# Kernel tuning notes

Measured on AMD Instinct MI355X. Metric: run time of the kernel, lower is better.

Reference implementation:

```python
import jax, jax.numpy as jnp
import numpy as np

N_HEADS, N_LEVELS, N_POINTS = 8, 4, 4
D_MODEL, D_FFN = 256, 2048
NQ, BS = 900, 4
SPATIAL = np.array([[128, 128], [64, 64], [32, 32], [16, 16]], dtype=np.int64)
HW = int((SPATIAL[:, 0] * SPATIAL[:, 1]).sum())


def _ln(x, g, b):
    mu = x.mean(-1, keepdims=True)
    var = x.var(-1, keepdims=True)
    return (x - mu) / jnp.sqrt(var + 1e-5) * g + b


def _lin(x, w, b):
    return x @ w.T + b


def _msdeform_attn(query, refp, mem, ss, starts, so_w, so_b, aw_w, aw_b, vp_w, vp_b, op_w, op_b):
    # query: (bs, nq, d), refp: (bs, nq, L, 2) in [0,1], mem: (bs, hw, d)
    bs, nq, d = query.shape
    hd = d // N_HEADS
    value = _lin(mem, vp_w, vp_b).reshape(bs, -1, N_HEADS, hd)  # (bs, hw, H, hd)
    offsets = _lin(query, so_w, so_b).reshape(bs, nq, N_HEADS, N_LEVELS, N_POINTS, 2)
    aw = _lin(query, aw_w, aw_b).reshape(bs, nq, N_HEADS, N_LEVELS * N_POINTS)
    aw = jax.nn.softmax(aw, axis=-1).reshape(bs, nq, N_HEADS, N_LEVELS, N_POINTS)
    # offset normalizer is (W, H) per level
    normalizer = jnp.asarray(ss[:, ::-1].copy(), dtype=query.dtype)  # (L, 2)
    loc = refp[:, :, None, :, None, :] + offsets / normalizer[None, None, None, :, None, :]
    out = jnp.zeros((bs, nq, N_HEADS, hd), dtype=query.dtype)
    for l in range(N_LEVELS):
        h_l, w_l = int(ss[l, 0]), int(ss[l, 1])
        vl = value[:, starts[l]:starts[l] + h_l * w_l]  # (bs, h*w, H, hd)
        # grid_sample align_corners=False: pixel coord = loc*size - 0.5
        x = loc[:, :, :, l, :, 0] * w_l - 0.5  # (bs, nq, H, P)
        y = loc[:, :, :, l, :, 1] * h_l - 0.5
        x0 = jnp.floor(x)
        y0 = jnp.floor(y)
        fx = x - x0
        fy = y - y0

        def gather(ix, iy, wgt):
            valid = (ix >= 0) & (ix < w_l) & (iy >= 0) & (iy < h_l)
            idx = (jnp.clip(iy, 0, h_l - 1) * w_l + jnp.clip(ix, 0, w_l - 1)).astype(jnp.int32)
            # (bs, nq, H, P) -> (bs, nq*P, H) to match vl's (bs, hw, H, hd)
            idxt = idx.transpose(0, 1, 3, 2).reshape(bs, nq * N_POINTS, N_HEADS)
            g = jnp.take_along_axis(vl, idxt[..., None], axis=1)  # (bs, nq*P, H, hd)
            g = g.reshape(bs, nq, N_POINTS, N_HEADS, hd).transpose(0, 1, 3, 2, 4)
            return g * (wgt * valid)[..., None]

        x0i = x0.astype(jnp.int32)
        y0i = y0.astype(jnp.int32)
        sampled = (gather(x0i, y0i, (1 - fx) * (1 - fy))
                   + gather(x0i + 1, y0i, fx * (1 - fy))
                   + gather(x0i, y0i + 1, (1 - fx) * fy)
                   + gather(x0i + 1, y0i + 1, fx * fy))  # (bs, nq, H, P, hd)
        out = out + (sampled * aw[:, :, :, l, :, None]).sum(axis=3)
    return _lin(out.reshape(bs, nq, d), op_w, op_b)


def _fwd(tgt, query_pos, memory, ref_points,
         sa_in_w, sa_in_b, sa_out_w, sa_out_b,
         ln1_g, ln1_b, ln2_g, ln2_b, ln3_g, ln3_b,
         so_w, so_b, aw_w, aw_b, vp_w, vp_b, op_w, op_b,
         ff1_w, ff1_b, ff2_w, ff2_b, spatial_shapes, level_start_index):
    nq, bs, d = tgt.shape
    hd = d // N_HEADS
    ss = np.asarray(spatial_shapes)
    starts = np.asarray(level_start_index)
    # ---- self attention (q = k = tgt + pos, v = tgt) ----
    qk = tgt + query_pos
    q = _lin(qk, sa_in_w[:d], sa_in_b[:d]).reshape(nq, bs, N_HEADS, hd)
    k = _lin(qk, sa_in_w[d:2 * d], sa_in_b[d:2 * d]).reshape(nq, bs, N_HEADS, hd)
    v = _lin(tgt, sa_in_w[2 * d:], sa_in_b[2 * d:]).reshape(nq, bs, N_HEADS, hd)
    scores = jnp.einsum('qbhd,kbhd->bhqk', q, k) / np.sqrt(hd).astype(tgt.dtype)
    attn = jax.nn.softmax(scores, axis=-1)
    sa = jnp.einsum('bhqk,kbhd->qbhd', attn, v).reshape(nq, bs, d)
    sa = _lin(sa, sa_out_w, sa_out_b)
    tgt = _ln(tgt + sa, ln2_g, ln2_b)
    # ---- deformable cross attention ----
    ca = _msdeform_attn((tgt + query_pos).transpose(1, 0, 2),
                        ref_points.transpose(1, 0, 2, 3),
                        memory.transpose(1, 0, 2), ss, starts,
                        so_w, so_b, aw_w, aw_b, vp_w, vp_b, op_w, op_b)
    tgt = _ln(tgt + ca.transpose(1, 0, 2), ln1_g, ln1_b)
    # ---- FFN ----
    ff = _lin(jax.nn.relu(_lin(tgt, ff1_w, ff1_b)), ff2_w, ff2_b)
    return _ln(tgt + ff, ln3_g, ln3_b)


def setup_inputs() -> dict:
    key = jax.random.key(0)
    ks = iter(jax.random.split(key, 32))
    d, dffn = D_MODEL, D_FFN
    nofs = N_HEADS * N_LEVELS * N_POINTS
    w = lambda *s: jax.random.normal(next(ks), s, dtype=jnp.float32) * 0.02
    starts = np.concatenate([[0], np.cumsum(SPATIAL[:, 0] * SPATIAL[:, 1])[:-1]]).astype(np.int64)
    return {
        'tgt': jax.random.normal(next(ks), (NQ, BS, d), dtype=jnp.float32),
        'query_pos': jax.random.normal(next(ks), (NQ, BS, d), dtype=jnp.float32),
        'memory': jax.random.normal(next(ks), (HW, BS, d), dtype=jnp.float32),
        'ref_points': jax.random.uniform(next(ks), (NQ, BS, N_LEVELS, 2), dtype=jnp.float32),
        'sa_in_w': w(3 * d, d), 'sa_in_b': w(3 * d), 'sa_out_w': w(d, d), 'sa_out_b': w(d),
        'ln1_g': jnp.ones((d,)), 'ln1_b': jnp.zeros((d,)),
        'ln2_g': jnp.ones((d,)), 'ln2_b': jnp.zeros((d,)),
        'ln3_g': jnp.ones((d,)), 'ln3_b': jnp.zeros((d,)),
        'so_w': w(nofs * 2, d), 'so_b': jax.random.normal(next(ks), (nofs * 2,), dtype=jnp.float32) * 0.5,
        'aw_w': w(nofs, d), 'aw_b': w(nofs),
        'vp_w': w(d, d), 'vp_b': w(d), 'op_w': w(d, d), 'op_b': w(d),
        'ff1_w': w(dffn, d), 'ff1_b': w(dffn), 'ff2_w': w(d, dffn), 'ff2_b': w(d),
        'spatial_shapes': SPATIAL, 'level_start_index': starts,
    }


def reference(tgt, query_pos, memory, ref_points, sa_in_w, sa_in_b, sa_out_w, sa_out_b, ln1_g, ln1_b, ln2_g, ln2_b, ln3_g, ln3_b, so_w, so_b, aw_w, aw_b, vp_w, vp_b, op_w, op_b, ff1_w, ff1_b, ff2_w, ff2_b, spatial_shapes, level_start_index):
    return _fwd(tgt, query_pos, memory, ref_points, sa_in_w, sa_in_b, sa_out_w, sa_out_b,
                ln1_g, ln1_b, ln2_g, ln2_b, ln3_g, ln3_b, so_w, so_b, aw_w, aw_b,
                vp_w, vp_b, op_w, op_b, ff1_w, ff1_b, ff2_w, ff2_b,
                spatial_shapes, level_start_index)
```

## Files before the change

kernel.cpp:

```cpp
#include <hip/hip_runtime.h>
#include <hip/hip_bf16.h>

#define D_MODEL 256
#define N_HEADS 8
#define HD 32
#define NQ 900
#define BS 4
#define MROWS (NQ * BS)
#define HW_TOT 21760
#define VROWS (HW_TOT * BS)

typedef __attribute__((ext_vector_type(8))) short bf16x8;
typedef __attribute__((ext_vector_type(4))) float f32x4;

__device__ inline short f2b(float f) {
  union { __hip_bfloat16 h; short s; } u;
  u.h = __float2bfloat16(f);
  return u.s;
}
__device__ inline float bu2f(unsigned short u) {
  union { unsigned int i; float f; } c;
  c.i = ((unsigned int)u) << 16;
  return c.f;
}
__device__ inline bf16x8 bzero8() {
  bf16x8 v;
#pragma unroll
  for (int j = 0; j < 8; ++j) v[j] = 0;
  return v;
}
__device__ inline f32x4 fzero4() {
  f32x4 v;
#pragma unroll
  for (int j = 0; j < 4; ++j) v[j] = 0.f;
  return v;
}

#define GLL16(gsrc, ldst)                                                     \
  __builtin_amdgcn_global_load_lds(                                           \
      (__attribute__((address_space(1))) void*)(gsrc),                        \
      (__attribute__((address_space(3))) void*)(ldst), 16, 0, 0)

__global__ __launch_bounds__(256) void prep_all(const float* __restrict__ s0,
                                                const float* __restrict__ s1,
                                                const float* __restrict__ s2,
                                                const float* __restrict__ s3,
                                                const float* __restrict__ s4,
                                                const float* __restrict__ s5,
                                                const float* __restrict__ s6,
                                                const float* __restrict__ s7,
                                                short* __restrict__ dst,
                                                const float* __restrict__ tgt,
                                                const float* __restrict__ qpos,
                                                short* __restrict__ tgtb,
                                                short* __restrict__ qkb,
                                                const float* __restrict__ so_b,
                                                const float* __restrict__ aw_b,
                                                float* __restrict__ biasSOAW) {
  int i = blockIdx.x * 256 + threadIdx.x;
  if (i < 1540096) {
    const float* s; int off;
    if (i < 196608)      { s = s0; off = 0; }
    else if (i < 262144) { s = s1; off = 196608; }
    else if (i < 327680) { s = s2; off = 262144; }
    else if (i < 360448) { s = s3; off = 327680; }
    else if (i < 425984) { s = s4; off = 360448; }
    else if (i < 491520) { s = s5; off = 425984; }
    else if (i < 1015808){ s = s6; off = 491520; }
    else                 { s = s7; off = 1015808; }
    dst[i] = f2b(s[i - off]);
  } else {
    int j = i - 1540096;
    float t = tgt[j], p = qpos[j];
    tgtb[j] = f2b(t);
    qkb[j] = f2b(t + p);
    if (j < 384) biasSOAW[j] = (j < 256) ? so_b[j] : aw_b[j - 256];
  }
}

template <int BN, int AF32, int OUTF32, int RELU>
__device__ __forceinline__ void gemm_core(const void* __restrict__ Xv,
                                          const short* __restrict__ W,
                                          const float* __restrict__ bias,
                                          void* __restrict__ outv,
                                          int M, int N, int K, int m0, int n0,
                                          int t0, int t1, int addBias,
                                          short* __restrict__ smem) {
  constexpr int NF = BN / 16;
  short* sA = smem;
  short* sB = smem + 2 * 2048;
  const int tid = threadIdx.x;
  const int wave = tid >> 6, lane = tid & 63;
  const int l15 = lane & 15, l4 = lane >> 4;
  const int wr = wave * 16;
  const float* Xf = (const float*)Xv;
  const short* Xh = (const short*)Xv;

  f32x4 acc[NF];
#pragma unroll
  for (int f = 0; f < NF; ++f) acc[f] = fzero4();

  const int alr = wave * 16 + (lane >> 2);
  const int ags = (lane & 3) ^ ((alr >> 1) & 3);
  const int arow = tid >> 2, ak = tid & 3;
  const int agsrc = ak ^ ((arow >> 1) & 3);
  float4 ra0, ra1;

  auto stageB = [&](int t, int buf) {
    short* bb = sB + buf * BN * 32;
#pragma unroll
    for (int j = 0; j < BN / 64; ++j) {
      int lr = j * 64 + alr;
      int gs = (lane & 3) ^ ((lr >> 1) & 3);
      const short* src = W + (size_t)(n0 + lr) * K + t * 32 + gs * 8;
      GLL16(src, bb + (j * 64 + wave * 16) * 32);
    }
  };
  auto stageA_gll = [&](int t, int buf) {
    const short* src = Xh + (size_t)(m0 + alr) * K + t * 32 + ags * 8;
    GLL16(src, sA + buf * 2048 + wave * 512);
  };
  auto loadA_f32 = [&](int t) {
    const float* p = Xf + (size_t)(m0 + arow) * K + t * 32 + agsrc * 8;
    ra0 = *reinterpret_cast<const float4*>(p);
    ra1 = *reinterpret_cast<const float4*>(p + 4);
  };
  auto writeA_f32 = [&](int buf) {
    bf16x8 v;
    v[0] = f2b(ra0.x); v[1] = f2b(ra0.y); v[2] = f2b(ra0.z); v[3] = f2b(ra0.w);
    v[4] = f2b(ra1.x); v[5] = f2b(ra1.y); v[6] = f2b(ra1.z); v[7] = f2b(ra1.w);
    *reinterpret_cast<bf16x8*>(&sA[buf * 2048 + arow * 32 + ak * 8]) = v;
  };
  auto compute = [&](int buf) {
    const int r = wr + l15;
    bf16x8 av = *reinterpret_cast<const bf16x8*>(
        &sA[buf * 2048 + r * 32 + ((l4 ^ ((r >> 1) & 3)) * 8)]);
#pragma unroll
    for (int f = 0; f < NF; ++f) {
      const int rb = f * 16 + l15;
      bf16x8 bv = *reinterpret_cast<const bf16x8*>(
          &sB[buf * BN * 32 + rb * 32 + ((l4 ^ ((rb >> 1) & 3)) * 8)]);
      acc[f] = __builtin_amdgcn_mfma_f32_16x16x32_bf16(av, bv, acc[f], 0, 0, 0);
    }
  };

  if constexpr (AF32) { loadA_f32(t0); writeA_f32(0); }
  else stageA_gll(t0, 0);
  stageB(t0, 0);
  __syncthreads();

  int buf = 0;
  for (int t = t0; t < t1; ++t) {
    if (t + 1 < t1) {
      if constexpr (AF32) loadA_f32(t + 1);
      else stageA_gll(t + 1, buf ^ 1);
      stageB(t + 1, buf ^ 1);
    }
    compute(buf);
    if (AF32 && t + 1 < t1) writeA_f32(buf ^ 1);
    __syncthreads();
    buf ^= 1;
  }

#pragma unroll
  for (int f = 0; f < NF; ++f) {
    int col = n0 + f * 16 + l15;
    float bfv = addBias ? bias[col] : 0.f;
#pragma unroll
    for (int i = 0; i < 4; ++i) {
      int row = m0 + wr + l4 * 4 + i;
      if (row >= M) continue;
      float v = acc[f][i] + bfv;
      if (RELU) v = fmaxf(v, 0.f);
      if constexpr (OUTF32)
        ((float*)outv)[(size_t)row * N + col] = v;
      else
        ((short*)outv)[(size_t)row * N + col] = f2b(v);
    }
  }
}

template <int BN, int AF32, int OUTF32, int RELU>
__global__ __launch_bounds__(256) void gemm2(const void* __restrict__ Xv,
                                             const short* __restrict__ W,
                                             const float* __restrict__ bias,
                                             void* __restrict__ outv,
                                             int M, int N, int K) {
  __shared__ __align__(16) short smem[2 * 2048 + 2 * BN * 32];
  gemm_core<BN, AF32, OUTF32, RELU>(Xv, W, bias, outv, M, N, K,
                                    blockIdx.x * 64, blockIdx.y * BN,
                                    0, K / 32, 1, smem);
}

__global__ __launch_bounds__(256) void gemm_splitk(const void* __restrict__ Xv,
                                                   const short* __restrict__ W,
                                                   const float* __restrict__ bias,
                                                   float* __restrict__ outp,
                                                   int M, int N, int K) {
  __shared__ __align__(16) short smem[2 * 2048 + 2 * 64 * 32];
  const int kc = blockIdx.z;
  const int ntc = K / 32 / 4;
  gemm_core<64, 0, 1, 0>(Xv, W, bias, outp + (size_t)kc * M * N, M, N, K,
                         blockIdx.x * 64, blockIdx.y * 64,
                         kc * ntc, (kc + 1) * ntc, kc == 0, smem);
}

__global__ __launch_bounds__(256) void qkv_gemm(const short* __restrict__ qkb,
                                                const short* __restrict__ tgtb,
                                                const short* __restrict__ Wqkv,
                                                const float* __restrict__ sa_in_b,
                                                short* __restrict__ QKb,
                                                short* __restrict__ Vb) {
  __shared__ __align__(16) short smem[2 * 2048 + 2 * 64 * 32];
  int bx = blockIdx.x;
  if (bx < 456) {
    gemm_core<64, 0, 0, 0>(qkb, Wqkv, sa_in_b, QKb, MROWS, 512, 256,
                           (bx % 57) * 64, (bx / 57) * 64, 0, 8, 1, smem);
  } else {
    bx -= 456;
    gemm_core<64, 0, 0, 0>(tgtb, Wqkv + 512 * 256, sa_in_b + 512, Vb, MROWS, 256, 256,
                           (bx % 57) * 64, (bx / 57) * 64, 0, 8, 1, smem);
  }
}

__device__ __forceinline__ void flash_body(const short* __restrict__ QK,
                                           const short* __restrict__ V,
                                           short* __restrict__ O,
                                           int bid, short* __restrict__ smem) {
  const int bh = bid & 31, b = bh >> 3, h = bh & 7;
  const int q0 = (bid >> 5) * 64;
  const int tid = threadIdx.x, wave = tid >> 6, lane = tid & 63;
  const int l15 = lane & 15, l4 = lane >> 4;
  const int cb = h * 32;

  short* sQ = smem;
  short* sK = smem + 2560;
  short* sVt = smem + 5120;
  short* sP = smem + 7424;

  {
    int row = tid >> 2, kof = (tid & 3) * 8;
    int q = q0 + row;
    bf16x8 v = (q < NQ) ? *reinterpret_cast<const bf16x8*>(QK + (size_t)(q * 4 + b) * 512 + cb + kof)
                        : bzero8();
    *reinterpret_cast<bf16x8*>(&sQ[row * 40 + kof]) = v;
  }
  __syncthreads();
  const int wr = wave * 16;
  const bf16x8 aq = *reinterpret_cast<bf16x8*>(&sQ[(wr + l15) * 40 + l4 * 8]);

  float mrow[4], lrow[4];
#pragma unroll
  for (int i = 0; i < 4; ++i) { mrow[i] = -1e30f; lrow[i] = 0.f; }
  f32x4 accO[2];
  accO[0] = fzero4(); accO[1] = fzero4();

  const int pswz = (((wr >> 2) + l4) & 3) << 3;
  const int pswzr = (((wr >> 2) + (l15 >> 2)) & 3) << 3;

  for (int kt = 0; kt < 15; ++kt) {
    const int k0 = kt * 64;
    {
      int row = tid >> 2, kof = (tid & 3) * 8;
      int kk = k0 + row;
      bf16x8 v = (kk < NQ)
          ? *reinterpret_cast<const bf16x8*>(QK + (size_t)(kk * 4 + b) * 512 + 256 + cb + kof)
          : bzero8();
      *reinterpret_cast<bf16x8*>(&sK[row * 40 + kof]) = v;
    }
    {
      int row = tid >> 2, dof = (tid & 3) * 8;
      int kk = k0 + row;
      bf16x8 vv = (kk < NQ)
          ? *reinterpret_cast<const bf16x8*>(V + (size_t)(kk * 4 + b) * 256 + cb + dof)
          : bzero8();
      const int kp = row ^ (((dof >> 3) & 3) << 4);
#pragma unroll
      for (int j = 0; j < 8; ++j) sVt[(dof + j) * 72 + kp] = vv[j];
    }
    __syncthreads();

    f32x4 s[4];
#pragma unroll
    for (int f = 0; f < 4; ++f) {
      bf16x8 bk = *reinterpret_cast<bf16x8*>(&sK[(f * 16 + l15) * 40 + l4 * 8]);
      s[f] = __builtin_amdgcn_mfma_f32_16x16x32_bf16(aq, bk, fzero4(), 0, 0, 0);
    }
#pragma unroll
    for (int f = 0; f < 4; ++f) {
      bool valid = (k0 + f * 16 + l15) < NQ;
#pragma unroll
      for (int i = 0; i < 4; ++i) {
        float sv = s[f][i] * 0.17677669529663687f;
        s[f][i] = valid ? sv : -1e30f;
      }
    }
    float mx[4];
#pragma unroll
    for (int i = 0; i < 4; ++i)
      mx[i] = fmaxf(fmaxf(s[0][i], s[1][i]), fmaxf(s[2][i], s[3][i]));
#pragma unroll
    for (int off = 1; off < 16; off <<= 1)
#pragma unroll
      for (int i = 0; i < 4; ++i) mx[i] = fmaxf(mx[i], __shfl_xor(mx[i], off));

    float alpha[4], rs[4];
#pragma unroll
    for (int i = 0; i < 4; ++i) {
      float mn = fmaxf(mrow[i], mx[i]);
      alpha[i] = __expf(mrow[i] - mn);
      mrow[i] = mn;
      rs[i] = 0.f;
    }
#pragma unroll
    for (int f = 0; f < 4; ++f)
#pragma unroll
      for (int i = 0; i < 4; ++i) {
        float p = __expf(s[f][i] - mrow[i]);
        rs[i] += p;
        sP[(wr + l4 * 4 + i) * 72 + ((f * 16 + l15) ^ pswz)] = f2b(p);
      }
#pragma unroll
    for (int off = 1; off < 16; off <<= 1)
#pragma unroll
      for (int i = 0; i < 4; ++i) rs[i] += __shfl_xor(rs[i], off);
#pragma unroll
    for (int i = 0; i < 4; ++i) lrow[i] = lrow[i] * alpha[i] + rs[i];
#pragma unroll
    for (int nf = 0; nf < 2; ++nf)
#pragma unroll
      for (int i = 0; i < 4; ++i) accO[nf][i] *= alpha[i];

#pragma unroll
    for (int ks = 0; ks < 2; ++ks) {
      bf16x8 ap = *reinterpret_cast<bf16x8*>(&sP[(wr + l15) * 72 + ((ks * 32 + l4 * 8) ^ pswzr)]);
#pragma unroll
      for (int nf = 0; nf < 2; ++nf) {
        const int d = nf * 16 + l15;
        const int kb = (ks * 32 + l4 * 8) ^ (((d >> 3) & 3) << 4);
        bf16x8 bv = *reinterpret_cast<bf16x8*>(&sVt[d * 72 + kb]);
        accO[nf] = __builtin_amdgcn_mfma_f32_16x16x32_bf16(ap, bv, accO[nf], 0, 0, 0);
      }
    }
    __syncthreads();
  }

#pragma unroll
  for (int nf = 0; nf < 2; ++nf)
#pragma unroll
    for (int i = 0; i < 4; ++i) {
      int q = q0 + wr + l4 * 4 + i;
      if (q < NQ)
        O[(size_t)(q * 4 + b) * 256 + cb + nf * 16 + l15] = f2b(accO[nf][i] / lrow[i]);
    }
}

__global__ __launch_bounds__(256) void flash_value(const short* __restrict__ QKb,
                                                   const short* __restrict__ Vb,
                                                   short* __restrict__ Ob,
                                                   const float* __restrict__ memory,
                                                   const short* __restrict__ Wvp,
                                                   const float* __restrict__ vp_b,
                                                   short* __restrict__ value) {
  __shared__ __align__(16) short smem[2 * 2048 + 2 * 128 * 32];
  int bx = blockIdx.x;
  if (bx < 480) {
    flash_body(QKb, Vb, Ob, bx, smem);
  } else {
    bx -= 480;
    gemm_core<128, 1, 0, 0>(memory, Wvp, vp_b, value, VROWS, 256, 256,
                            (bx >> 1) * 64, (bx & 1) * 128, 0, 8, 1, smem);
  }
}

__global__ __launch_bounds__(256) void ln_kernel(const float* __restrict__ A,
                                                 const float* __restrict__ B,
                                                 const float* __restrict__ g,
                                                 const float* __restrict__ bb,
                                                 float* __restrict__ outF,
                                                 short* __restrict__ outB,
                                                 const float* __restrict__ addv) {
  const int row = blockIdx.x;
  const int t = threadIdx.x;
  const size_t base = (size_t)row * D_MODEL;
  float x = A[base + t] + B[base + t];
  float s = x, s2 = x * x;
#pragma unroll
  for (int off = 32; off; off >>= 1) {
    s += __shfl_xor(s, off);
    s2 += __shfl_xor(s2, off);
  }
  __shared__ float wsum[4], wsum2[4];
  const int w = t >> 6;
  if ((t & 63) == 0) { wsum[w] = s; wsum2[w] = s2; }
  __syncthreads();
  s = wsum[0] + wsum[1] + wsum[2] + wsum[3];
  s2 = wsum2[0] + wsum2[1] + wsum2[2] + wsum2[3];
  const float mu = s * (1.f / 256.f);
  const float var = s2 * (1.f / 256.f) - mu * mu;
  const float inv = rsqrtf(var + 1e-5f);
  float y = (x - mu) * inv * g[t] + bb[t];
  outF[base + t] = y;
  if (outB) outB[base + t] = f2b(y + (addv ? addv[base + t] : 0.f));
}

__global__ __launch_bounds__(256) void ln4_kernel(const float* __restrict__ A,
                                                  const float* __restrict__ P,
                                                  const float* __restrict__ g,
                                                  const float* __restrict__ bb,
                                                  float* __restrict__ outF) {
  const int row = blockIdx.x;
  const int t = threadIdx.x;
  const size_t base = (size_t)row * D_MODEL + t;
  const size_t stride = (size_t)MROWS * D_MODEL;
  float x = A[base] + P[base] + P[base + stride] + P[base + 2 * stride] + P[base + 3 * stride];
  float s = x, s2 = x * x;
#pragma unroll
  for (int off = 32; off; off >>= 1) {
    s += __shfl_xor(s, off);
    s2 += __shfl_xor(s2, off);
  }
  __shared__ float wsum[4], wsum2[4];
  const int w = t >> 6;
  if ((t & 63) == 0) { wsum[w] = s; wsum2[w] = s2; }
  __syncthreads();
  s = wsum[0] + wsum[1] + wsum[2] + wsum[3];
  s2 = wsum2[0] + wsum2[1] + wsum2[2] + wsum2[3];
  const float mu = s * (1.f / 256.f);
  const float var = s2 * (1.f / 256.f) - mu * mu;
  const float inv = rsqrtf(var + 1e-5f);
  outF[base] = (x - mu) * inv * g[t] + bb[t];
}

__global__ __launch_bounds__(256) void msds_kernel(const unsigned short* __restrict__ value,
                                                   const float* __restrict__ soaw,
                                                   const float* __restrict__ refp,
                                                   unsigned short* __restrict__ out) {
  const int tid = threadIdx.x;
  const int row = blockIdx.x * 4 + (tid >> 6);
  const int col4 = tid & 63;
  const int h = col4 >> 3;
  const int dp = (col4 & 7) * 4;
  const int b = row & 3;

  const int WL[4] = {128, 64, 32, 16};
  const int ST[4] = {0, 16384, 20480, 21504};

  const float* awp = soaw + (size_t)row * 384 + 256 + h * 16;
  float awv[16];
  float m = -1e30f;
#pragma unroll
  for (int i = 0; i < 16; ++i) { awv[i] = awp[i]; m = fmaxf(m, awv[i]); }
  float s = 0.f;
#pragma unroll
  for (int i = 0; i < 16; ++i) { awv[i] = __expf(awv[i] - m); s += awv[i]; }
  const float invs = 1.f / s;

  const float* offp = soaw + (size_t)row * 384 + h * 32;
  float acc0 = 0.f, acc1 = 0.f, acc2 = 0.f, acc3 = 0.f;
#pragma unroll
  for (int l = 0; l < 4; ++l) {
    const int wl = WL[l], hl = WL[l], st = ST[l];
    const float rx = refp[((size_t)row * 4 + l) * 2 + 0];
    const float ry = refp[((size_t)row * 4 + l) * 2 + 1];
#pragma unroll
    for (int p = 0; p < 4; ++p) {
      const float ox = offp[l * 8 + p * 2 + 0];
      const float oy = offp[l * 8 + p * 2 + 1];
      const float x = (rx + ox / (float)wl) * (float)wl - 0.5f;
      const float y = (ry + oy / (float)hl) * (float)hl - 0.5f;
      const float x0f = floorf(x), y0f = floorf(y);
      const int x0 = (int)x0f, y0 = (int)y0f;
      const float fx = x - x0f, fy = y - y0f;
      const float a = awv[l * 4 + p] * invs;
      const float w00 = (1.f - fx) * (1.f - fy);
      const float w10 = fx * (1.f - fy);
      const float w01 = (1.f - fx) * fy;
      const float w11 = fx * fy;
      float s0 = 0.f, s1 = 0.f, s2 = 0.f, s3 = 0.f;
      auto gat = [&](int ix, int iy, float wgt) {
        if (ix >= 0 && ix < wl && iy >= 0 && iy < hl) {
          const unsigned short* p2 =
              value + ((size_t)((st + iy * wl + ix) * 4 + b)) * 256 + h * 32 + dp;
          ushort4 u = *reinterpret_cast<const ushort4*>(p2);
          s0 += wgt * bu2f(u.x);
          s1 += wgt * bu2f(u.y);
          s2 += wgt * bu2f(u.z);
          s3 += wgt * bu2f(u.w);
        }
      };
      gat(x0, y0, w00);
      gat(x0 + 1, y0, w10);
      gat(x0, y0 + 1, w01);
      gat(x0 + 1, y0 + 1, w11);
      acc0 += a * s0; acc1 += a * s1; acc2 += a * s2; acc3 += a * s3;
    }
  }
  ushort4 o;
  o.x = (unsigned short)f2b(acc0);
  o.y = (unsigned short)f2b(acc1);
  o.z = (unsigned short)f2b(acc2);
  o.w = (unsigned short)f2b(acc3);
  *reinterpret_cast<ushort4*>(&out[(size_t)row * 256 + h * 32 + dp]) = o;
}

extern "C" void kernel_launch(void* const* d_in, const int* in_sizes, int n_in,
                              void* d_out, int out_size, void* d_ws, size_t ws_size,
                              hipStream_t stream) {
  const float* tgt      = (const float*)d_in[0];
  const float* qpos     = (const float*)d_in[1];
  const float* memory   = (const float*)d_in[2];
  const float* refp     = (const float*)d_in[3];
  const float* sa_in_w  = (const float*)d_in[4];
  const float* sa_in_b  = (const float*)d_in[5];
  const float* sa_out_w = (const float*)d_in[6];
  const float* sa_out_b = (const float*)d_in[7];
  const float* ln1_g = (const float*)d_in[8];
  const float* ln1_b = (const float*)d_in[9];
  const float* ln2_g = (const float*)d_in[10];
  const float* ln2_b = (const float*)d_in[11];
  const float* ln3_g = (const float*)d_in[12];
  const float* ln3_b = (const float*)d_in[13];
  const float* so_w = (const float*)d_in[14];
  const float* so_b = (const float*)d_in[15];
  const float* aw_w = (const float*)d_in[16];
  const float* aw_b = (const float*)d_in[17];
  const float* vp_w = (const float*)d_in[18];
  const float* vp_b = (const float*)d_in[19];
  const float* op_w = (const float*)d_in[20];
  const float* op_b = (const float*)d_in[21];
  const float* ff1_w = (const float*)d_in[22];
  const float* ff1_b = (const float*)d_in[23];
  const float* ff2_w = (const float*)d_in[24];
  const float* ff2_b = (const float*)d_in[25];

  float* out = (float*)d_out;
  float* ws = (float*)d_ws;

  short* Wb       = (short*)ws;
  float* biasSOAW = ws + 770048;
  short* tgtb   = (short*)(ws + 770432);
  short* qkb    = (short*)(ws + 1231232);
  short* QKb    = (short*)(ws + 1692032);
  short* Vb     = (short*)(ws + 2613632);
  short* Ob     = (short*)(ws + 3074432);
  float* SA     = ws + 3535232;
  float* F      = ws + 4456832;
  short* qk2b   = (short*)(ws + 5378432);
  float* SOAW   = ws + 5839232;
  short* value  = (short*)(ws + 7221632);
  short* sampled= (short*)(ws + 18362752);
  float* CA     = ws + 18823552;
  float* tgt3   = ws + 19745152;
  short* tgt3b  = (short*)(ws + 20666752);
  short* H      = (short*)(ws + 21127552);
  float* FFp    = ws + 7221632;

  const short* Wqkv = Wb;
  const short* Wsa  = Wb + 196608;
  const short* Wso  = Wb + 262144;
  const short* Wvp  = Wb + 360448;
  const short* Wop  = Wb + 425984;
  const short* Wff1 = Wb + 491520;
  const short* Wff2 = Wb + 1015808;

  prep_all<<<9616, 256, 0, stream>>>(sa_in_w, sa_out_w, so_w, aw_w, vp_w, op_w,
                                     ff1_w, ff2_w, Wb, tgt, qpos, tgtb, qkb,
                                     so_b, aw_b, biasSOAW);
  qkv_gemm<<<684, 256, 0, stream>>>(qkb, tgtb, Wqkv, sa_in_b, QKb, Vb);
  flash_value<<<3200, 256, 0, stream>>>(QKb, Vb, Ob, memory, Wvp, vp_b, value);
  gemm2<64, 0, 1, 0><<<dim3(57, 4), 256, 0, stream>>>(Ob, Wsa, sa_out_b, SA, MROWS, 256, 256);
  ln_kernel<<<MROWS, 256, 0, stream>>>(tgt, SA, ln2_g, ln2_b, F, qk2b, qpos);
  gemm2<64, 0, 1, 0><<<dim3(57, 6), 256, 0, stream>>>(qk2b, Wso, biasSOAW, SOAW, MROWS, 384, 256);
  msds_kernel<<<900, 256, 0, stream>>>((const unsigned short*)value, SOAW, refp,
                                       (unsigned short*)sampled);
  gemm2<64, 0, 1, 0><<<dim3(57, 4), 256, 0, stream>>>(sampled, Wop, op_b, CA, MROWS, 256, 256);
  ln_kernel<<<MROWS, 256, 0, stream>>>(F, CA, ln1_g, ln1_b, tgt3, tgt3b, nullptr);
  gemm2<64, 0, 0, 1><<<dim3(57, 32), 256, 0, stream>>>(tgt3b, Wff1, ff1_b, H, MROWS, 2048, 256);
  gemm_splitk<<<dim3(57, 4, 4), 256, 0, stream>>>(H, Wff2, ff2_b, FFp, MROWS, 256, 2048);
  ln4_kernel<<<MROWS, 256, 0, stream>>>(tgt3, FFp, ln3_g, ln3_b, out);
}
```

Before: 177.8 us.

## Replace LDS-tiled value projection GEMM with register-resident full-K MFMA per wave

The value projection that runs alongside flash attention no longer uses the shared-memory tiled gemm_core. Each wave now loads a 16-row strip of memory with the full K=256, converts it to bf16 in registers, and computes all 256 output columns with MFMA, streaming the weight fragments straight from global memory. This removes LDS staging and barriers and halves the GEMM block count (2720 to 1360). The cost is heavy register pressure (16 accumulators plus 8 A fragments), which may limit occupancy, and repeated uncoalesced weight reads from L2.

```diff
diff --git a/kernel.cpp b/kernel.cpp
--- a/kernel.cpp
+++ b/kernel.cpp
@@ -355,6 +355,47 @@
     }
 }
 
+__device__ __forceinline__ void value_body(const float* __restrict__ memory,
+                                           const short* __restrict__ Wvp,
+                                           const float* __restrict__ vp_b,
+                                           short* __restrict__ value, int vb) {
+  const int tid = threadIdx.x;
+  const int wave = tid >> 6, lane = tid & 63;
+  const int l15 = lane & 15, l4 = lane >> 4;
+  const int m0 = (vb * 4 + wave) * 16;
+
+  bf16x8 af[8];
+#pragma unroll
+  for (int k = 0; k < 8; ++k) {
+    const float* p = memory + (size_t)(m0 + l15) * 256 + k * 32 + l4 * 8;
+    float4 x = *reinterpret_cast<const float4*>(p);
+    float4 y = *reinterpret_cast<const float4*>(p + 4);
+    bf16x8 v;
+    v[0] = f2b(x.x); v[1] = f2b(x.y); v[2] = f2b(x.z); v[3] = f2b(x.w);
+    v[4] = f2b(y.x); v[5] = f2b(y.y); v[6] = f2b(y.z); v[7] = f2b(y.w);
+    af[k] = v;
+  }
+  f32x4 acc[16];
+#pragma unroll
+  for (int f = 0; f < 16; ++f) acc[f] = fzero4();
+#pragma unroll
+  for (int k = 0; k < 8; ++k) {
+#pragma unroll
+    for (int f = 0; f < 16; ++f) {
+      bf16x8 bv = *reinterpret_cast<const bf16x8*>(
+          Wvp + (size_t)(f * 16 + l15) * 256 + k * 32 + l4 * 8);
+      acc[f] = __builtin_amdgcn_mfma_f32_16x16x32_bf16(af[k], bv, acc[f], 0, 0, 0);
+    }
+  }
+#pragma unroll
+  for (int f = 0; f < 16; ++f) {
+    float bb = vp_b[f * 16 + l15];
+#pragma unroll
+    for (int i = 0; i < 4; ++i)
+      value[(size_t)(m0 + l4 * 4 + i) * 256 + f * 16 + l15] = f2b(acc[f][i] + bb);
+  }
+}
+
 __global__ __launch_bounds__(256) void flash_value(const short* __restrict__ QKb,
                                                    const short* __restrict__ Vb,
                                                    short* __restrict__ Ob,
@@ -362,14 +403,12 @@
                                                    const short* __restrict__ Wvp,
                                                    const float* __restrict__ vp_b,
                                                    short* __restrict__ value) {
-  __shared__ __align__(16) short smem[2 * 2048 + 2 * 128 * 32];
+  __shared__ __align__(16) short smem[12288];
   int bx = blockIdx.x;
   if (bx < 480) {
     flash_body(QKb, Vb, Ob, bx, smem);
   } else {
-    bx -= 480;
-    gemm_core<128, 1, 0, 0>(memory, Wvp, vp_b, value, VROWS, 256, 256,
-                            (bx >> 1) * 64, (bx & 1) * 128, 0, 8, 1, smem);
+    value_body(memory, Wvp, vp_b, value, bx - 480);
   }
 }
 
@@ -568,7 +607,7 @@
                                      ff1_w, ff2_w, Wb, tgt, qpos, tgtb, qkb,
                                      so_b, aw_b, biasSOAW);
   qkv_gemm<<<684, 256, 0, stream>>>(qkb, tgtb, Wqkv, sa_in_b, QKb, Vb);
-  flash_value<<<3200, 256, 0, stream>>>(QKb, Vb, Ob, memory, Wvp, vp_b, value);
+  flash_value<<<1840, 256, 0, stream>>>(QKb, Vb, Ob, memory, Wvp, vp_b, value);
   gemm2<64, 0, 1, 0><<<dim3(57, 4), 256, 0, stream>>>(Ob, Wsa, sa_out_b, SA, MROWS, 256, 256);
   ln_kernel<<<MROWS, 256, 0, stream>>>(tgt, SA, ln2_g, ln2_b, F, qk2b, qpos);
   gemm2<64, 0, 1, 0><<<dim3(57, 6), 256, 0, stream>>>(qk2b, Wso, biasSOAW, SOAW, MROWS, 384, 256);
```

Result: slower. 252.7 us (+42.1%).

## Double-buffer K/V tiles in flash attention with async global-to-LDS K loads

Applied to the files above, without the earlier changes.

The self-attention flash kernel now double-buffers the K and transposed-V tiles in shared memory. The next K tile is issued via direct global-to-LDS loads and the next V tile is prefetched into registers while the current tile's QK and PV MFMAs run, which removes one barrier per iteration. Q/K LDS layout changes to a 32-wide XOR-swizzled form suitable for the direct loads. Shared memory grows, which may reduce occupancy for the fused flash/value-projection kernel. K loads for rows past NQ are no longer zero-guarded and rely on masking of those scores instead.

```diff
diff --git a/kernel.cpp b/kernel.cpp
--- a/kernel.cpp
+++ b/kernel.cpp
@@ -234,20 +234,45 @@
   const int cb = h * 32;
 
   short* sQ = smem;
-  short* sK = smem + 2560;
-  short* sVt = smem + 5120;
-  short* sP = smem + 7424;
+  short* sK = smem + 2048;
+  short* sVt = smem + 6144;
+  short* sP = smem + 10752;
+
+  const int sr = wave * 16 + (lane >> 2);
+  const int sgs = (lane & 3) ^ (sr & 3);
+
+  auto stageK = [&](int kt, int buf) {
+    const short* src = QK + (size_t)((kt * 64 + sr) * 4 + b) * 512 + 256 + cb + sgs * 8;
+    GLL16(src, sK + buf * 2048 + wave * 512);
+  };
+  const int vrow = tid >> 2, vdof = (tid & 3) * 8;
+  const int vkp = vrow ^ (((vdof >> 3) & 3) << 4);
+  auto loadV = [&](int kt) -> bf16x8 {
+    int kk = kt * 64 + vrow;
+    return (kk < NQ)
+        ? *reinterpret_cast<const bf16x8*>(V + (size_t)(kk * 4 + b) * 256 + cb + vdof)
+        : bzero8();
+  };
+  auto writeV = [&](bf16x8 vv, int buf) {
+    short* dst = sVt + buf * 2304;
+#pragma unroll
+    for (int j = 0; j < 8; ++j) dst[(vdof + j) * 72 + vkp] = vv[j];
+  };
 
   {
-    int row = tid >> 2, kof = (tid & 3) * 8;
-    int q = q0 + row;
-    bf16x8 v = (q < NQ) ? *reinterpret_cast<const bf16x8*>(QK + (size_t)(q * 4 + b) * 512 + cb + kof)
-                        : bzero8();
-    *reinterpret_cast<bf16x8*>(&sQ[row * 40 + kof]) = v;
+    const short* qsrc = QK + (size_t)((q0 + sr) * 4 + b) * 512 + cb + sgs * 8;
+    GLL16(qsrc, sQ + wave * 512);
+  }
+  stageK(0, 0);
+  {
+    bf16x8 v0 = loadV(0);
+    writeV(v0, 0);
   }
   __syncthreads();
+
   const int wr = wave * 16;
-  const bf16x8 aq = *reinterpret_cast<bf16x8*>(&sQ[(wr + l15) * 40 + l4 * 8]);
+  const int rq = wr + l15;
+  const bf16x8 aq = *reinterpret_cast<const bf16x8*>(&sQ[rq * 32 + ((l4 ^ (rq & 3)) * 8)]);
 
   float mrow[4], lrow[4];
 #pragma unroll
@@ -260,30 +285,20 @@
 
   for (int kt = 0; kt < 15; ++kt) {
     const int k0 = kt * 64;
-    {
-      int row = tid >> 2, kof = (tid & 3) * 8;
-      int kk = k0 + row;
-      bf16x8 v = (kk < NQ)
-          ? *reinterpret_cast<const bf16x8*>(QK + (size_t)(kk * 4 + b) * 512 + 256 + cb + kof)
-          : bzero8();
-      *reinterpret_cast<bf16x8*>(&sK[row * 40 + kof]) = v;
-    }
-    {
-      int row = tid >> 2, dof = (tid & 3) * 8;
-      int kk = k0 + row;
-      bf16x8 vv = (kk < NQ)
-          ? *reinterpret_cast<const bf16x8*>(V + (size_t)(kk * 4 + b) * 256 + cb + dof)
-          : bzero8();
-      const int kp = row ^ (((dof >> 3) & 3) << 4);
-#pragma unroll
-      for (int j = 0; j < 8; ++j) sVt[(dof + j) * 72 + kp] = vv[j];
-    }
-    __syncthreads();
+    const int buf = kt & 1;
+    const bool more = (kt + 1 < 15);
+    bf16x8 vnext = bzero8();
+    if (more) {
+      stageK(kt + 1, buf ^ 1);
+      vnext = loadV(kt + 1);
+    }
 
     f32x4 s[4];
 #pragma unroll
     for (int f = 0; f < 4; ++f) {
-      bf16x8 bk = *reinterpret_cast<bf16x8*>(&sK[(f * 16 + l15) * 40 + l4 * 8]);
+      const int rb = f * 16 + l15;
+      bf16x8 bk = *reinterpret_cast<bf16x8*>(
+          &sK[buf * 2048 + rb * 32 + ((l4 ^ (rb & 3)) * 8)]);
       s[f] = __builtin_amdgcn_mfma_f32_16x16x32_bf16(aq, bk, fzero4(), 0, 0, 0);
     }
 #pragma unroll
@@ -333,15 +348,17 @@
 
 #pragma unroll
     for (int ks = 0; ks < 2; ++ks) {
-      bf16x8 ap = *reinterpret_cast<bf16x8*>(&sP[(wr + l15) * 72 + ((ks * 32 + l4 * 8) ^ pswzr)]);
+      bf16x8 ap = *reinterpret_cast<bf16x8*>(
+          &sP[(wr + l15) * 72 + ((ks * 32 + l4 * 8) ^ pswzr)]);
 #pragma unroll
       for (int nf = 0; nf < 2; ++nf) {
         const int d = nf * 16 + l15;
         const int kb = (ks * 32 + l4 * 8) ^ (((d >> 3) & 3) << 4);
-        bf16x8 bv = *reinterpret_cast<bf16x8*>(&sVt[d * 72 + kb]);
+        bf16x8 bv = *reinterpret_cast<bf16x8*>(&sVt[buf * 2304 + d * 72 + kb]);
         accO[nf] = __builtin_amdgcn_mfma_f32_16x16x32_bf16(ap, bv, accO[nf], 0, 0, 0);
       }
     }
+    if (more) writeV(vnext, buf ^ 1);
     __syncthreads();
   }
 
@@ -362,7 +379,7 @@
                                                    const short* __restrict__ Wvp,
                                                    const float* __restrict__ vp_b,
                                                    short* __restrict__ value) {
-  __shared__ __align__(16) short smem[2 * 2048 + 2 * 128 * 32];
+  __shared__ __align__(16) short smem[15360];
   int bx = blockIdx.x;
   if (bx < 480) {
     flash_body(QKb, Vb, Ob, bx, smem);
```

Measured after the change: 175.4 us. Within noise of the previous version (-1.4%).
